# Kernel optimization log

Hardware: AMD Instinct MI355X
Metric: run time of the kernel (lower is better)

## Reference

```python
import jax, jax.numpy as jnp
import numpy as np

B, SQ, SE = 16, 1024, 1024
C_IN, C_ENC, DK, DV, H = 256, 256, 64, 64, 8
BN_EPS = 1e-5
NEG_SLOPE = 0.01  # torch LeakyReLU default


def setup_inputs() -> dict:
    key = jax.random.key(0)
    ks = jax.random.split(key, 8)
    x = jax.random.normal(ks[0], (B, SE, C_ENC), dtype=jnp.float32)
    q = jax.random.normal(ks[1], (B, SQ, C_IN), dtype=jnp.float32)
    # per-head 1x1-conv projection weights, stacked over heads
    Wq = jax.random.normal(ks[2], (H, DK, C_IN), dtype=jnp.float32) / np.sqrt(C_IN)
    Wk = jax.random.normal(ks[3], (H, DK, C_ENC), dtype=jnp.float32) / np.sqrt(C_ENC)
    Wv = jax.random.normal(ks[4], (H, DV, C_ENC), dtype=jnp.float32) / np.sqrt(C_ENC)
    # output projection (Conv1d(H*DV -> C_IN, k=1, bias=False))
    Wp = jax.random.normal(ks[5], (C_IN, H * DV), dtype=jnp.float32) / np.sqrt(H * DV)
    gamma = jax.random.normal(ks[6], (C_IN,), dtype=jnp.float32) * 0.1 + 1.0
    beta = jax.random.normal(ks[7], (C_IN,), dtype=jnp.float32) * 0.1
    return {"x": x, "q": q, "Wq": Wq, "Wk": Wk, "Wv": Wv, "Wp": Wp,
            "gamma": gamma, "beta": beta}


def reference(x, q, Wq, Wk, Wv, Wp, gamma, beta):
    # per-head Q/K/V via 1x1 conv == einsum over channel dim
    qh = jnp.einsum('bsc,hdc->bhsd', q, Wq)   # [B,H,SQ,DK]
    kh = jnp.einsum('btc,hdc->bhtd', x, Wk)   # [B,H,SE,DK]
    vh = jnp.einsum('btc,hec->bhte', x, Wv)   # [B,H,SE,DV]
    scale = 1.0 / jnp.sqrt(jnp.asarray(DK, dtype=qh.dtype))
    scores = jnp.einsum('bhsd,bhtd->bhst', qh, kh) * scale  # [B,H,SQ,SE]
    attn = jax.nn.softmax(scores, axis=-1)
    oh = jnp.einsum('bhst,bhte->bhse', attn, vh)  # [B,H,SQ,DV]
    # concat heads along feature dim (head-major order, as torch.cat over dim=2)
    o = jnp.transpose(oh, (0, 2, 1, 3)).reshape(B, SQ, H * DV)
    # LBRD projection: 1x1 conv -> BatchNorm1d (train mode: batch stats) -> LeakyReLU
    p = jnp.einsum('bsf,cf->bsc', o, Wp)  # [B,SQ,C_IN]
    mean = jnp.mean(p, axis=(0, 1))        # per-channel over (B, L)
    var = jnp.var(p, axis=(0, 1))          # biased, matching torch BN normalization
    y = (p - mean) * jax.lax.rsqrt(var + BN_EPS) * gamma + beta
    return jnp.where(y >= 0, y, NEG_SLOPE * y)
```

## Files before the change

### kernel.cpp

```cpp
#include <hip/hip_runtime.h>
#include <cstddef>

#define B_    16
#define SQ_   1024
#define SE_   1024
#define CIN_  256
#define DK_   64
#define H_    8
#define HD_   512
#define NROWS 16384
#define BN_EPS 1e-5f
#define NEG_SLOPE 0.01f

typedef __attribute__((ext_vector_type(8))) short bf16x8;
typedef __attribute__((ext_vector_type(4))) float f32x4;

#define BAR()        __builtin_amdgcn_s_barrier()
#define WAIT_LGKM0() asm volatile("s_waitcnt lgkmcnt(0)" ::: "memory")

__device__ __forceinline__ unsigned short f2bf(float f) {
    unsigned int u = __float_as_uint(f);
    return (unsigned short)((u + 0x7FFFu + ((u >> 16) & 1u)) >> 16);
}

#if __has_builtin(__builtin_amdgcn_perm)
__device__ __forceinline__ unsigned int pack_trunc(float lo, float hi) {
    return __builtin_amdgcn_perm(__float_as_uint(hi), __float_as_uint(lo), 0x07060302u);
}
#else
__device__ __forceinline__ unsigned int pack_trunc(float lo, float hi) {
    return (__float_as_uint(lo) >> 16) | (__float_as_uint(hi) & 0xFFFF0000u);
}
#endif

#if __has_builtin(__builtin_amdgcn_exp2f)
#define EXP2F(x) __builtin_amdgcn_exp2f(x)
#else
#define EXP2F(x) exp2f(x)
#endif

__device__ __forceinline__ ushort4 pack4(f32x4 v) {
    ushort4 p;
    p.x = f2bf(v[0]); p.y = f2bf(v[1]);
    p.z = f2bf(v[2]); p.w = f2bf(v[3]);
    return p;
}

__device__ __forceinline__ bf16x8 cvt8(float4 f0, float4 f1) {
    uint4 pk;
    pk.x = pack_trunc(f0.x, f0.y);
    pk.y = pack_trunc(f0.z, f0.w);
    pk.z = pack_trunc(f1.x, f1.y);
    pk.w = pack_trunc(f1.z, f1.w);
    return *(bf16x8*)&pk;
}

__global__ __launch_bounds__(256) void wcast(const float* __restrict__ Wq,
                                             const float* __restrict__ Wk,
                                             const float* __restrict__ Wv,
                                             const float* __restrict__ Wp,
                                             unsigned short* __restrict__ dWq,
                                             unsigned short* __restrict__ dWkv,
                                             unsigned short* __restrict__ dWp,
                                             float* __restrict__ stats) {
    if (blockIdx.x < 2) stats[blockIdx.x * 256 + threadIdx.x] = 0.f;
    int i = blockIdx.x * 256 + threadIdx.x;
    int which = i >> 15, off = i & 32767;
    const float* s; unsigned short* d; float sc = 1.0f;
    if (which == 0)      { s = Wq; d = dWq; sc = 0.18033688011112042f; }
    else if (which == 1) { s = Wk; d = dWkv; }
    else if (which == 2) { s = Wv; d = dWkv + 131072; }
    else                 { s = Wp; d = dWp; }
    float4 v = *(const float4*)(s + (size_t)off * 4);
    ushort4 pk;
    pk.x = f2bf(v.x * sc); pk.y = f2bf(v.y * sc);
    pk.z = f2bf(v.z * sc); pk.w = f2bf(v.w * sc);
    *(ushort4*)(d + (size_t)off * 4) = pk;
}

__global__ __launch_bounds__(256) void gemm_qkv9(const float* __restrict__ qsrc,
                                                 const float* __restrict__ xsrc,
                                                 const unsigned short* __restrict__ Wqb,
                                                 const unsigned short* __restrict__ Wkvb,
                                                 unsigned short* __restrict__ qh,
                                                 unsigned short* __restrict__ khb,
                                                 unsigned short* __restrict__ vTb) {
    __shared__ __align__(16) unsigned short smem[32768];
    unsigned short* Ws = smem;
    unsigned short* Cs = smem;

    const int tid = threadIdx.x;
    const int w = tid >> 6, l = tid & 63, lq = l >> 4, lr = l & 15;

    const int flat = blockIdx.x;
    const int xcd  = flat & 7;
    const int jj   = flat >> 3;
    const int bx   = jj % 12;
    const int by   = (jj / 12) + xcd * 16;

    const bool isQ = bx < 4;
    const bool isV = bx >= 8;
    const float* A = isQ ? qsrc : xsrc;
    const unsigned short* W = isQ ? Wqb : Wkvb;
    const int n0 = (isQ ? bx : bx - 4) * 128;
    const int m0 = by * 128;

    f32x4 acc[2][8] = {};
    float4 aA[8], aB[8];

    const float* A0 = A + (size_t)(m0 + w * 32 + lr) * 256 + lq * 8;
    const float* A1 = A + (size_t)(m0 + w * 32 + 16 + lr) * 256 + lq * 8;

#define LOAD_A(buf, kstep) do {                                              \
        buf[0] = *(const float4*)(A0 + (kstep) * 64);                        \
        buf[1] = *(const float4*)(A0 + (kstep) * 64 + 4);                    \
        buf[2] = *(const float4*)(A0 + (kstep) * 64 + 32);                   \
        buf[3] = *(const float4*)(A0 + (kstep) * 64 + 36);                   \
        buf[4] = *(const float4*)(A1 + (kstep) * 64);                        \
        buf[5] = *(const float4*)(A1 + (kstep) * 64 + 4);                    \
        buf[6] = *(const float4*)(A1 + (kstep) * 64 + 32);                   \
        buf[7] = *(const float4*)(A1 + (kstep) * 64 + 36);                   \
    } while (0)

#define QKV_STEP(buf, kstep) do {                                            \
        _Pragma("unroll")                                                    \
        for (int ks = 0; ks < 2; ++ks) {                                     \
            bf16x8 a0 = cvt8(buf[ks * 2], buf[ks * 2 + 1]);                  \
            bf16x8 a1 = cvt8(buf[4 + ks * 2], buf[4 + ks * 2 + 1]);          \
            const int colu = (kstep) * 8 + ks * 4 + lq;                      \
            const int cswz = colu ^ (lr & 7);                                \
            if (!isV) {                                                      \
                _Pragma("unroll")                                            \
                for (int j = 0; j < 8; ++j) {                                \
                    bf16x8 bb = *(bf16x8*)&Ws[((j * 16 + lr) * 32 + cswz) * 8]; \
                    acc[0][j] = __builtin_amdgcn_mfma_f32_16x16x32_bf16(bb, a0, acc[0][j], 0, 0, 0); \
                    acc[1][j] = __builtin_amdgcn_mfma_f32_16x16x32_bf16(bb, a1, acc[1][j], 0, 0, 0); \
                }                                                            \
            } else {                                                         \
                _Pragma("unroll")                                            \
                for (int j = 0; j < 8; ++j) {                                \
                    bf16x8 bb = *(bf16x8*)&Ws[((j * 16 + lr) * 32 + cswz) * 8]; \
                    acc[0][j] = __builtin_amdgcn_mfma_f32_16x16x32_bf16(a0, bb, acc[0][j], 0, 0, 0); \
                    acc[1][j] = __builtin_amdgcn_mfma_f32_16x16x32_bf16(a1, bb, acc[1][j], 0, 0, 0); \
                }                                                            \
            }                                                                \
        }                                                                    \
    } while (0)

    LOAD_A(aA, 0);

    #pragma unroll
    for (int i = 0; i < 16; ++i) {
        int u = tid + i * 256;
        int row = u >> 5, colu = u & 31;
        uint4 v = *(const uint4*)(W + (size_t)(n0 + row) * 256 + colu * 8);
        *(uint4*)&Ws[(row * 32 + (colu ^ (row & 7))) * 8] = v;
    }
    __syncthreads();

    LOAD_A(aB, 1);
    QKV_STEP(aA, 0);
    LOAD_A(aA, 2);
    QKV_STEP(aB, 1);
    LOAD_A(aB, 3);
    QKV_STEP(aA, 2);
    QKV_STEP(aB, 3);

#undef LOAD_A
#undef QKV_STEP

    __syncthreads();
    const int c16 = tid & 15;
    const int rb  = tid >> 4;
    if (!isV) {
        #pragma unroll
        for (int mf = 0; mf < 2; ++mf)
            #pragma unroll
            for (int j = 0; j < 8; ++j)
                *(ushort4*)&Cs[(w * 32 + mf * 16 + lr) * 144 + j * 16 + lq * 4] =
                    pack4(acc[mf][j]);
        __syncthreads();
        unsigned short* C = isQ ? qh : khb;
        #pragma unroll
        for (int it = 0; it < 8; ++it) {
            int r = it * 16 + rb;
            *(uint4*)(C + (size_t)(m0 + r) * 512 + n0 + c16 * 8) =
                *(const uint4*)(Cs + r * 144 + c16 * 8);
        }
    } else {
        #pragma unroll
        for (int mf = 0; mf < 2; ++mf)
            #pragma unroll
            for (int j = 0; j < 8; ++j)
                *(ushort4*)&Cs[(j * 16 + lr) * 144 + w * 32 + mf * 16 + lq * 4] =
                    pack4(acc[mf][j]);
        __syncthreads();
        const int bb = m0 >> 10, t0 = m0 & 1023;
        #pragma unroll
        for (int it = 0; it < 8; ++it) {
            int el = it * 16 + rb;
            int colv = n0 - 512 + el;
            int hh = colv >> 6, e = colv & 63;
            *(uint4*)(vTb + (size_t)((bb * 8 + hh) * 64 + e) * 1024 + t0 + c16 * 8) =
                *(const uint4*)(Cs + el * 144 + c16 * 8);
        }
    }
}

__global__ __launch_bounds__(256, 4) void attn_mfma13(const unsigned short* __restrict__ qh,
                                                      const unsigned short* __restrict__ kh,
                                                      const unsigned short* __restrict__ vT,
                                                      unsigned short* __restrict__ o) {
    __shared__ __align__(16) unsigned short Ks[64 * 64];
    __shared__ __align__(16) unsigned short Vs[64 * 64];
    __shared__ __align__(16) unsigned short Ps[4][32 * 40];

    const int tid = threadIdx.x;
    const int w = tid >> 6, l = tid & 63, lq = l >> 4, lr = l & 15;

    const int flat = blockIdx.x;
    const int xcd  = flat & 7;
    const int jj   = flat >> 3;
    const int q0   = (jj & 7) * 128;
    const int hb   = (jj >> 3) + xcd * 16;
    const int h    = hb & 7;
    const int b    = hb >> 3;

    const int swz = (lr & 7) << 3;

    bf16x8 qf[2][2];
    #pragma unroll
    for (int mm = 0; mm < 2; ++mm) {
        const unsigned short* qr =
            qh + (size_t)(b * SQ_ + q0 + w * 32 + mm * 16 + lr) * HD_ + h * DK_;
        qf[mm][0] = *(const bf16x8*)(qr + lq * 8);
        qf[mm][1] = *(const bf16x8*)(qr + 32 + lq * 8);
    }

    const unsigned short* kb = kh + (size_t)(b * SE_) * HD_ + h * DK_;
    const unsigned short* vb = vT + (size_t)((b * 8 + h) * 64) * 1024;

    const int se = tid >> 3;
    const int sc = (tid & 7) * 8;
    const int sswz = (se & 7) << 3;

    float l_i[2] = {};
    f32x4 oacc[2][4] = {};
    unsigned short* Pw = Ps[w];

    uint4 kR[2], vR[2];
    #pragma unroll
    for (int ps = 0; ps < 2; ++ps) {
        int rr = se + ps * 32;
        kR[ps] = *(const uint4*)(kb + (size_t)rr * HD_ + sc);
        vR[ps] = *(const uint4*)(vb + (size_t)rr * 1024 + sc);
    }

    for (int t0 = 0; t0 < SE_; t0 += 64) {
        BAR();
        #pragma unroll
        for (int ps = 0; ps < 2; ++ps) {
            int rr = se + ps * 32;
            int ad = ((rr * 64 + sc) ^ sswz);
            *(uint4*)&Ks[ad] = kR[ps];
            *(uint4*)&Vs[ad] = vR[ps];
        }
        if (t0 + 64 < SE_) {
            #pragma unroll
            for (int ps = 0; ps < 2; ++ps) {
                int rr = se + ps * 32;
                kR[ps] = *(const uint4*)(kb + (size_t)(t0 + 64 + rr) * HD_ + sc);
                vR[ps] = *(const uint4*)(vb + (size_t)rr * 1024 + t0 + 64 + sc);
            }
        }
        WAIT_LGKM0();
        BAR();

        f32x4 s0[2][2] = {};
        __builtin_amdgcn_s_setprio(1);
        #pragma unroll
        for (int ks = 0; ks < 2; ++ks)
            #pragma unroll
            for (int tt = 0; tt < 2; ++tt) {
                bf16x8 kf = *(bf16x8*)&Ks[((tt * 16 + lr) * 64 + ks * 32 + lq * 8) ^ swz];
                #pragma unroll
                for (int mm = 0; mm < 2; ++mm)
                    s0[tt][mm] = __builtin_amdgcn_mfma_f32_16x16x32_bf16(kf, qf[mm][ks], s0[tt][mm], 0, 0, 0);
            }
        __builtin_amdgcn_s_setprio(0);

        #pragma unroll
        for (int mm = 0; mm < 2; ++mm)
            #pragma unroll
            for (int tt = 0; tt < 2; ++tt) {
                float e0 = EXP2F(s0[tt][mm][0]);
                float e1 = EXP2F(s0[tt][mm][1]);
                float e2 = EXP2F(s0[tt][mm][2]);
                float e3 = EXP2F(s0[tt][mm][3]);
                l_i[mm] += (e0 + e1) + (e2 + e3);
                uint2 pk;
                pk.x = pack_trunc(e0, e1);
                pk.y = pack_trunc(e2, e3);
                *(uint2*)&Pw[(mm * 16 + lr) * 40 + tt * 16 + lq * 4] = pk;
            }

        f32x4 s1[2][2] = {};
        __builtin_amdgcn_s_setprio(1);
        #pragma unroll
        for (int ks = 0; ks < 2; ++ks)
            #pragma unroll
            for (int tt = 0; tt < 2; ++tt) {
                bf16x8 kf = *(bf16x8*)&Ks[(((tt + 2) * 16 + lr) * 64 + ks * 32 + lq * 8) ^ swz];
                #pragma unroll
                for (int mm = 0; mm < 2; ++mm)
                    s1[tt][mm] = __builtin_amdgcn_mfma_f32_16x16x32_bf16(kf, qf[mm][ks], s1[tt][mm], 0, 0, 0);
            }
        __builtin_amdgcn_s_setprio(0);

        asm volatile("s_waitcnt lgkmcnt(0)" ::: "memory");

        __builtin_amdgcn_s_setprio(1);
        {
            bf16x8 pf[2];
            #pragma unroll
            for (int mm = 0; mm < 2; ++mm)
                pf[mm] = *(bf16x8*)&Pw[(mm * 16 + lr) * 40 + lq * 8];
            #pragma unroll
            for (int j = 0; j < 4; ++j) {
                bf16x8 vf = *(bf16x8*)&Vs[((j * 16 + lr) * 64 + lq * 8) ^ swz];
                #pragma unroll
                for (int mm = 0; mm < 2; ++mm)
                    oacc[mm][j] = __builtin_amdgcn_mfma_f32_16x16x32_bf16(vf, pf[mm], oacc[mm][j], 0, 0, 0);
            }
        }
        __builtin_amdgcn_s_setprio(0);

        #pragma unroll
        for (int mm = 0; mm < 2; ++mm)
            #pragma unroll
            for (int tt = 0; tt < 2; ++tt) {
                float e0 = EXP2F(s1[tt][mm][0]);
                float e1 = EXP2F(s1[tt][mm][1]);
                float e2 = EXP2F(s1[tt][mm][2]);
                float e3 = EXP2F(s1[tt][mm][3]);
                l_i[mm] += (e0 + e1) + (e2 + e3);
                uint2 pk;
                pk.x = pack_trunc(e0, e1);
                pk.y = pack_trunc(e2, e3);
                *(uint2*)&Pw[(mm * 16 + lr) * 40 + tt * 16 + lq * 4] = pk;
            }

        asm volatile("s_waitcnt lgkmcnt(0)" ::: "memory");

        __builtin_amdgcn_s_setprio(1);
        {
            bf16x8 pf[2];
            #pragma unroll
            for (int mm = 0; mm < 2; ++mm)
                pf[mm] = *(bf16x8*)&Pw[(mm * 16 + lr) * 40 + lq * 8];
            #pragma unroll
            for (int j = 0; j < 4; ++j) {
                bf16x8 vf = *(bf16x8*)&Vs[((j * 16 + lr) * 64 + 32 + lq * 8) ^ swz];
                #pragma unroll
                for (int mm = 0; mm < 2; ++mm)
                    oacc[mm][j] = __builtin_amdgcn_mfma_f32_16x16x32_bf16(vf, pf[mm], oacc[mm][j], 0, 0, 0);
            }
        }
        __builtin_amdgcn_s_setprio(0);
    }

    float inv[2];
    #pragma unroll
    for (int mm = 0; mm < 2; ++mm) {
        float t = l_i[mm];
        t += __shfl_xor(t, 16);
        t += __shfl_xor(t, 32);
        inv[mm] = 1.0f / t;
    }

    #pragma unroll
    for (int mm = 0; mm < 2; ++mm)
        #pragma unroll
        for (int j = 0; j < 4; ++j) {
            f32x4 v = oacc[mm][j];
            v[0] *= inv[mm]; v[1] *= inv[mm]; v[2] *= inv[mm]; v[3] *= inv[mm];
            *(ushort4*)&o[(size_t)(b * SQ_ + q0 + w * 32 + mm * 16 + lr) * HD_ +
                          h * DK_ + j * 16 + lq * 4] = pack4(v);
        }
}

__global__ __launch_bounds__(256) void gemm_out2(const unsigned short* __restrict__ A,
                                                 const unsigned short* __restrict__ W,
                                                 float* __restrict__ C,
                                                 float* __restrict__ gsum,
                                                 float* __restrict__ gsumsq) {
    __shared__ __align__(16) unsigned short As[128 * 72];
    __shared__ __align__(16) unsigned short Ws[64 * 72];
    const int tid = threadIdx.x;
    const int w = tid >> 6, l = tid & 63, lq = l >> 4, lr = l & 15;
    const int n0 = blockIdx.x * 64, m0 = blockIdx.y * 128;
    const int K = 512;

    const int arow = tid >> 1, aoff = (tid & 1) * 32;
    const int wrow = tid >> 2, woff = (tid & 3) * 16;

    f32x4 acc[2][4] = {};
    uint4 aR[4], wR[2];

    {
        const unsigned short* Ar = A + (size_t)(m0 + arow) * K + aoff;
        #pragma unroll
        for (int c = 0; c < 4; ++c) aR[c] = *(const uint4*)(Ar + c * 8);
        const unsigned short* Wr = W + (size_t)(n0 + wrow) * K + woff;
        #pragma unroll
        for (int c = 0; c < 2; ++c) wR[c] = *(const uint4*)(Wr + c * 8);
    }

    for (int k0 = 0; k0 < K; k0 += 64) {
        BAR();
        #pragma unroll
        for (int c = 0; c < 4; ++c)
            *(uint4*)&As[arow * 72 + aoff + c * 8] = aR[c];
        #pragma unroll
        for (int c = 0; c < 2; ++c)
            *(uint4*)&Ws[wrow * 72 + woff + c * 8] = wR[c];

        if (k0 + 64 < K) {
            const unsigned short* Ar = A + (size_t)(m0 + arow) * K + k0 + 64 + aoff;
            #pragma unroll
            for (int c = 0; c < 4; ++c) aR[c] = *(const uint4*)(Ar + c * 8);
            const unsigned short* Wr = W + (size_t)(n0 + wrow) * K + k0 + 64 + woff;
            #pragma unroll
            for (int c = 0; c < 2; ++c) wR[c] = *(const uint4*)(Wr + c * 8);
        }
        WAIT_LGKM0();
        BAR();

        #pragma unroll
        for (int ks = 0; ks < 2; ++ks) {
            bf16x8 a0 = *(bf16x8*)&As[(w * 32 + lr) * 72 + ks * 32 + lq * 8];
            bf16x8 a1 = *(bf16x8*)&As[(w * 32 + 16 + lr) * 72 + ks * 32 + lq * 8];
            #pragma unroll
            for (int j = 0; j < 4; ++j) {
                bf16x8 bb = *(bf16x8*)&Ws[(j * 16 + lr) * 72 + ks * 32 + lq * 8];
                acc[0][j] = __builtin_amdgcn_mfma_f32_16x16x32_bf16(a0, bb, acc[0][j], 0, 0, 0);
                acc[1][j] = __builtin_amdgcn_mfma_f32_16x16x32_bf16(a1, bb, acc[1][j], 0, 0, 0);
            }
        }
    }

    float cs[4] = {}, cq[4] = {};
    #pragma unroll
    for (int m = 0; m < 2; ++m)
        #pragma unroll
        for (int j = 0; j < 4; ++j)
            #pragma unroll
            for (int r = 0; r < 4; ++r) {
                float v = acc[m][j][r];
                C[(size_t)(m0 + w * 32 + m * 16 + lq * 4 + r) * 256 + n0 + j * 16 + lr] = v;
                cs[j] += v;
                cq[j] += v * v;
            }
    #pragma unroll
    for (int j = 0; j < 4; ++j) {
        cs[j] += __shfl_xor(cs[j], 16); cs[j] += __shfl_xor(cs[j], 32);
        cq[j] += __shfl_xor(cq[j], 16); cq[j] += __shfl_xor(cq[j], 32);
    }
    __syncthreads();
    float* red = (float*)As;
    if (lq == 0) {
        #pragma unroll
        for (int j = 0; j < 4; ++j) {
            red[w * 128 + j * 16 + lr]      = cs[j];
            red[w * 128 + 64 + j * 16 + lr] = cq[j];
        }
    }
    __syncthreads();
    if (tid < 128) {
        int col = tid & 63, stat = tid >> 6;
        float t = red[stat * 64 + col] + red[128 + stat * 64 + col] +
                  red[256 + stat * 64 + col] + red[384 + stat * 64 + col];
        atomicAdd((stat ? gsumsq : gsum) + n0 + col, t);
    }
}

__global__ __launch_bounds__(256) void bn_norm4(const float* __restrict__ p,
                                                const float* __restrict__ gsum,
                                                const float* __restrict__ gsumsq,
                                                const float* __restrict__ gamma,
                                                const float* __restrict__ beta,
                                                float* __restrict__ out) {
    int i = blockIdx.x * 256 + threadIdx.x;
    int c0 = (i * 4) & 255;
    const float invN = 1.0f / (float)NROWS;
    float4 pv = *(const float4*)(p + (size_t)i * 4);
    float vals[4] = {pv.x, pv.y, pv.z, pv.w};
    float res[4];
    #pragma unroll
    for (int k = 0; k < 4; ++k) {
        int c = c0 + k;
        float mean = gsum[c] * invN;
        float var  = gsumsq[c] * invN - mean * mean;
        float v = (vals[k] - mean) * rsqrtf(var + BN_EPS) * gamma[c] + beta[c];
        res[k] = v >= 0.f ? v : NEG_SLOPE * v;
    }
    float4 ov = {res[0], res[1], res[2], res[3]};
    *(float4*)(out + (size_t)i * 4) = ov;
}

extern "C" void kernel_launch(void* const* d_in, const int* in_sizes, int n_in,
                              void* d_out, int out_size, void* d_ws, size_t ws_size,
                              hipStream_t stream) {
    const float* x     = (const float*)d_in[0];
    const float* q     = (const float*)d_in[1];
    const float* Wq    = (const float*)d_in[2];
    const float* Wk    = (const float*)d_in[3];
    const float* Wv    = (const float*)d_in[4];
    const float* Wp    = (const float*)d_in[5];
    const float* gamma = (const float*)d_in[6];
    const float* beta  = (const float*)d_in[7];
    float* out = (float*)d_out;

    char* base = (char*)d_ws;
    unsigned short* Wqb  = (unsigned short*)(base + 0);
    unsigned short* Wkvb = (unsigned short*)(base + 262144);
    unsigned short* Wpb  = (unsigned short*)(base + 786432);
    unsigned short* qh   = (unsigned short*)(base + 1048576);
    unsigned short* khb  = (unsigned short*)(base + 17825792);
    unsigned short* vTb  = (unsigned short*)(base + 34603008);
    unsigned short* ob   = (unsigned short*)(base + 51380224);
    float*          pbuf = (float*)        (base + 68157440);
    float*          stats= (float*)        (base + 84934656);

    wcast<<<512, 256, 0, stream>>>(Wq, Wk, Wv, Wp, Wqb, Wkvb, Wpb, stats);

    gemm_qkv9<<<1536, 256, 0, stream>>>(q, x, Wqb, Wkvb, qh, khb, vTb);

    attn_mfma13<<<1024, 256, 0, stream>>>(qh, khb, vTb, ob);

    gemm_out2<<<dim3(4, 128), 256, 0, stream>>>(ob, Wpb, pbuf, stats, stats + 256);

    bn_norm4<<<4096, 256, 0, stream>>>(pbuf, stats, stats + 256, gamma, beta, out);
}
```

Measured before the change: 222.9 us.

## Double the attention query tile with double-buffered K/V and rework the output GEMM

The attention kernel now gives each wave 64 query rows instead of 32 and launches 512 blocks instead of 1024, so each K/V tile loaded into LDS serves twice as many queries. K/V use double-buffered shared memory, which drops one barrier per iteration. The output GEMM keeps the whole 64x512 weight slice in swizzled LDS, loads A fragments straight from global into registers with ping-pong prefetch, and needs no per-k barriers. In exchange the attention kernel uses more registers and LDS and runs with fewer blocks, which can lower occupancy.

```diff
diff --git a/kernel.cpp b/kernel.cpp
--- a/kernel.cpp
+++ b/kernel.cpp
@@ -207,13 +207,13 @@
     }
 }
 
-__global__ __launch_bounds__(256, 4) void attn_mfma13(const unsigned short* __restrict__ qh,
-                                                      const unsigned short* __restrict__ kh,
-                                                      const unsigned short* __restrict__ vT,
-                                                      unsigned short* __restrict__ o) {
-    __shared__ __align__(16) unsigned short Ks[64 * 64];
-    __shared__ __align__(16) unsigned short Vs[64 * 64];
-    __shared__ __align__(16) unsigned short Ps[4][32 * 40];
+__global__ __launch_bounds__(256) void attn_mfma14(const unsigned short* __restrict__ qh,
+                                                   const unsigned short* __restrict__ kh,
+                                                   const unsigned short* __restrict__ vT,
+                                                   unsigned short* __restrict__ o) {
+    __shared__ __align__(16) unsigned short Ks[2][64 * 64];
+    __shared__ __align__(16) unsigned short Vs[2][64 * 64];
+    __shared__ __align__(16) unsigned short Ps[4][64 * 40];
 
     const int tid = threadIdx.x;
     const int w = tid >> 6, l = tid & 63, lq = l >> 4, lr = l & 15;
@@ -221,18 +221,18 @@
     const int flat = blockIdx.x;
     const int xcd  = flat & 7;
     const int jj   = flat >> 3;
-    const int q0   = (jj & 7) * 128;
-    const int hb   = (jj >> 3) + xcd * 16;
+    const int q0   = (jj & 3) * 256;
+    const int hb   = (jj >> 2) + xcd * 16;
     const int h    = hb & 7;
     const int b    = hb >> 3;
 
     const int swz = (lr & 7) << 3;
 
-    bf16x8 qf[2][2];
-    #pragma unroll
-    for (int mm = 0; mm < 2; ++mm) {
+    bf16x8 qf[4][2];
+    #pragma unroll
+    for (int mm = 0; mm < 4; ++mm) {
         const unsigned short* qr =
-            qh + (size_t)(b * SQ_ + q0 + w * 32 + mm * 16 + lr) * HD_ + h * DK_;
+            qh + (size_t)(b * SQ_ + q0 + w * 64 + mm * 16 + lr) * HD_ + h * DK_;
         qf[mm][0] = *(const bf16x8*)(qr + lq * 8);
         qf[mm][1] = *(const bf16x8*)(qr + 32 + lq * 8);
     }
@@ -244,8 +244,8 @@
     const int sc = (tid & 7) * 8;
     const int sswz = (se & 7) << 3;
 
-    float l_i[2] = {};
-    f32x4 oacc[2][4] = {};
+    float l_i[4] = {};
+    f32x4 oacc[4][4] = {};
     unsigned short* Pw = Ps[w];
 
     uint4 kR[2], vR[2];
@@ -255,42 +255,61 @@
         kR[ps] = *(const uint4*)(kb + (size_t)rr * HD_ + sc);
         vR[ps] = *(const uint4*)(vb + (size_t)rr * 1024 + sc);
     }
-
-    for (int t0 = 0; t0 < SE_; t0 += 64) {
-        BAR();
-        #pragma unroll
-        for (int ps = 0; ps < 2; ++ps) {
-            int rr = se + ps * 32;
-            int ad = ((rr * 64 + sc) ^ sswz);
-            *(uint4*)&Ks[ad] = kR[ps];
-            *(uint4*)&Vs[ad] = vR[ps];
-        }
-        if (t0 + 64 < SE_) {
+    #pragma unroll
+    for (int ps = 0; ps < 2; ++ps) {
+        int rr = se + ps * 32;
+        int ad = ((rr * 64 + sc) ^ sswz);
+        *(uint4*)&Ks[0][ad] = kR[ps];
+        *(uint4*)&Vs[0][ad] = vR[ps];
+    }
+    #pragma unroll
+    for (int ps = 0; ps < 2; ++ps) {
+        int rr = se + ps * 32;
+        kR[ps] = *(const uint4*)(kb + (size_t)(64 + rr) * HD_ + sc);
+        vR[ps] = *(const uint4*)(vb + (size_t)rr * 1024 + 64 + sc);
+    }
+    WAIT_LGKM0();
+    BAR();
+
+    for (int ti = 0; ti < 16; ++ti) {
+        unsigned short* Kc = Ks[ti & 1];
+        unsigned short* Vc = Vs[ti & 1];
+        if (ti + 1 < 16) {
+            unsigned short* Kn = Ks[(ti + 1) & 1];
+            unsigned short* Vn = Vs[(ti + 1) & 1];
             #pragma unroll
             for (int ps = 0; ps < 2; ++ps) {
                 int rr = se + ps * 32;
-                kR[ps] = *(const uint4*)(kb + (size_t)(t0 + 64 + rr) * HD_ + sc);
-                vR[ps] = *(const uint4*)(vb + (size_t)rr * 1024 + t0 + 64 + sc);
-            }
-        }
-        WAIT_LGKM0();
-        BAR();
-
-        f32x4 s0[2][2] = {};
+                int ad = ((rr * 64 + sc) ^ sswz);
+                *(uint4*)&Kn[ad] = kR[ps];
+                *(uint4*)&Vn[ad] = vR[ps];
+            }
+            if (ti + 2 < 16) {
+                int t2 = (ti + 2) * 64;
+                #pragma unroll
+                for (int ps = 0; ps < 2; ++ps) {
+                    int rr = se + ps * 32;
+                    kR[ps] = *(const uint4*)(kb + (size_t)(t2 + rr) * HD_ + sc);
+                    vR[ps] = *(const uint4*)(vb + (size_t)rr * 1024 + t2 + sc);
+                }
+            }
+        }
+
+        f32x4 s0[2][4] = {};
         __builtin_amdgcn_s_setprio(1);
         #pragma unroll
         for (int ks = 0; ks < 2; ++ks)
             #pragma unroll
             for (int tt = 0; tt < 2; ++tt) {
-                bf16x8 kf = *(bf16x8*)&Ks[((tt * 16 + lr) * 64 + ks * 32 + lq * 8) ^ swz];
+                bf16x8 kf = *(bf16x8*)&Kc[((tt * 16 + lr) * 64 + ks * 32 + lq * 8) ^ swz];
                 #pragma unroll
-                for (int mm = 0; mm < 2; ++mm)
+                for (int mm = 0; mm < 4; ++mm)
                     s0[tt][mm] = __builtin_amdgcn_mfma_f32_16x16x32_bf16(kf, qf[mm][ks], s0[tt][mm], 0, 0, 0);
             }
         __builtin_amdgcn_s_setprio(0);
 
         #pragma unroll
-        for (int mm = 0; mm < 2; ++mm)
+        for (int mm = 0; mm < 4; ++mm)
             #pragma unroll
             for (int tt = 0; tt < 2; ++tt) {
                 float e0 = EXP2F(s0[tt][mm][0]);
@@ -304,15 +323,15 @@
                 *(uint2*)&Pw[(mm * 16 + lr) * 40 + tt * 16 + lq * 4] = pk;
             }
 
-        f32x4 s1[2][2] = {};
+        f32x4 s1[2][4] = {};
         __builtin_amdgcn_s_setprio(1);
         #pragma unroll
         for (int ks = 0; ks < 2; ++ks)
             #pragma unroll
             for (int tt = 0; tt < 2; ++tt) {
-                bf16x8 kf = *(bf16x8*)&Ks[(((tt + 2) * 16 + lr) * 64 + ks * 32 + lq * 8) ^ swz];
+                bf16x8 kf = *(bf16x8*)&Kc[(((tt + 2) * 16 + lr) * 64 + ks * 32 + lq * 8) ^ swz];
                 #pragma unroll
-                for (int mm = 0; mm < 2; ++mm)
+                for (int mm = 0; mm < 4; ++mm)
                     s1[tt][mm] = __builtin_amdgcn_mfma_f32_16x16x32_bf16(kf, qf[mm][ks], s1[tt][mm], 0, 0, 0);
             }
         __builtin_amdgcn_s_setprio(0);
@@ -321,22 +340,22 @@
 
         __builtin_amdgcn_s_setprio(1);
         {
-            bf16x8 pf[2];
-            #pragma unroll
-            for (int mm = 0; mm < 2; ++mm)
+            bf16x8 pf[4];
+            #pragma unroll
+            for (int mm = 0; mm < 4; ++mm)
                 pf[mm] = *(bf16x8*)&Pw[(mm * 16 + lr) * 40 + lq * 8];
             #pragma unroll
             for (int j = 0; j < 4; ++j) {
-                bf16x8 vf = *(bf16x8*)&Vs[((j * 16 + lr) * 64 + lq * 8) ^ swz];
+                bf16x8 vf = *(bf16x8*)&Vc[((j * 16 + lr) * 64 + lq * 8) ^ swz];
                 #pragma unroll
-                for (int mm = 0; mm < 2; ++mm)
+                for (int mm = 0; mm < 4; ++mm)
                     oacc[mm][j] = __builtin_amdgcn_mfma_f32_16x16x32_bf16(vf, pf[mm], oacc[mm][j], 0, 0, 0);
             }
         }
         __builtin_amdgcn_s_setprio(0);
 
         #pragma unroll
-        for (int mm = 0; mm < 2; ++mm)
+        for (int mm = 0; mm < 4; ++mm)
             #pragma unroll
             for (int tt = 0; tt < 2; ++tt) {
                 float e0 = EXP2F(s1[tt][mm][0]);
@@ -354,24 +373,29 @@
 
         __builtin_amdgcn_s_setprio(1);
         {
-            bf16x8 pf[2];
-            #pragma unroll
-            for (int mm = 0; mm < 2; ++mm)
+            bf16x8 pf[4];
+            #pragma unroll
+            for (int mm = 0; mm < 4; ++mm)
                 pf[mm] = *(bf16x8*)&Pw[(mm * 16 + lr) * 40 + lq * 8];
             #pragma unroll
             for (int j = 0; j < 4; ++j) {
-                bf16x8 vf = *(bf16x8*)&Vs[((j * 16 + lr) * 64 + 32 + lq * 8) ^ swz];
+                bf16x8 vf = *(bf16x8*)&Vc[((j * 16 + lr) * 64 + 32 + lq * 8) ^ swz];
                 #pragma unroll
-                for (int mm = 0; mm < 2; ++mm)
+                for (int mm = 0; mm < 4; ++mm)
                     oacc[mm][j] = __builtin_amdgcn_mfma_f32_16x16x32_bf16(vf, pf[mm], oacc[mm][j], 0, 0, 0);
             }
         }
         __builtin_amdgcn_s_setprio(0);
-    }
-
-    float inv[2];
-    #pragma unroll
-    for (int mm = 0; mm < 2; ++mm) {
+
+        if (ti + 1 < 16) {
+            WAIT_LGKM0();
+            BAR();
+        }
+    }
+
+    float inv[4];
+    #pragma unroll
+    for (int mm = 0; mm < 4; ++mm) {
         float t = l_i[mm];
         t += __shfl_xor(t, 16);
         t += __shfl_xor(t, 32);
@@ -379,75 +403,78 @@
     }
 
     #pragma unroll
-    for (int mm = 0; mm < 2; ++mm)
+    for (int mm = 0; mm < 4; ++mm)
         #pragma unroll
         for (int j = 0; j < 4; ++j) {
             f32x4 v = oacc[mm][j];
             v[0] *= inv[mm]; v[1] *= inv[mm]; v[2] *= inv[mm]; v[3] *= inv[mm];
-            *(ushort4*)&o[(size_t)(b * SQ_ + q0 + w * 32 + mm * 16 + lr) * HD_ +
+            *(ushort4*)&o[(size_t)(b * SQ_ + q0 + w * 64 + mm * 16 + lr) * HD_ +
                           h * DK_ + j * 16 + lq * 4] = pack4(v);
         }
 }
 
-__global__ __launch_bounds__(256) void gemm_out2(const unsigned short* __restrict__ A,
+__global__ __launch_bounds__(256) void gemm_out3(const unsigned short* __restrict__ A,
                                                  const unsigned short* __restrict__ W,
                                                  float* __restrict__ C,
                                                  float* __restrict__ gsum,
                                                  float* __restrict__ gsumsq) {
-    __shared__ __align__(16) unsigned short As[128 * 72];
-    __shared__ __align__(16) unsigned short Ws[64 * 72];
+    __shared__ __align__(16) unsigned short Ws[32768];
     const int tid = threadIdx.x;
     const int w = tid >> 6, l = tid & 63, lq = l >> 4, lr = l & 15;
     const int n0 = blockIdx.x * 64, m0 = blockIdx.y * 128;
     const int K = 512;
 
-    const int arow = tid >> 1, aoff = (tid & 1) * 32;
-    const int wrow = tid >> 2, woff = (tid & 3) * 16;
-
     f32x4 acc[2][4] = {};
-    uint4 aR[4], wR[2];
-
-    {
-        const unsigned short* Ar = A + (size_t)(m0 + arow) * K + aoff;
-        #pragma unroll
-        for (int c = 0; c < 4; ++c) aR[c] = *(const uint4*)(Ar + c * 8);
-        const unsigned short* Wr = W + (size_t)(n0 + wrow) * K + woff;
-        #pragma unroll
-        for (int c = 0; c < 2; ++c) wR[c] = *(const uint4*)(Wr + c * 8);
-    }
-
-    for (int k0 = 0; k0 < K; k0 += 64) {
-        BAR();
-        #pragma unroll
-        for (int c = 0; c < 4; ++c)
-            *(uint4*)&As[arow * 72 + aoff + c * 8] = aR[c];
-        #pragma unroll
-        for (int c = 0; c < 2; ++c)
-            *(uint4*)&Ws[wrow * 72 + woff + c * 8] = wR[c];
-
-        if (k0 + 64 < K) {
-            const unsigned short* Ar = A + (size_t)(m0 + arow) * K + k0 + 64 + aoff;
-            #pragma unroll
-            for (int c = 0; c < 4; ++c) aR[c] = *(const uint4*)(Ar + c * 8);
-            const unsigned short* Wr = W + (size_t)(n0 + wrow) * K + k0 + 64 + woff;
-            #pragma unroll
-            for (int c = 0; c < 2; ++c) wR[c] = *(const uint4*)(Wr + c * 8);
-        }
-        WAIT_LGKM0();
-        BAR();
-
-        #pragma unroll
-        for (int ks = 0; ks < 2; ++ks) {
-            bf16x8 a0 = *(bf16x8*)&As[(w * 32 + lr) * 72 + ks * 32 + lq * 8];
-            bf16x8 a1 = *(bf16x8*)&As[(w * 32 + 16 + lr) * 72 + ks * 32 + lq * 8];
-            #pragma unroll
-            for (int j = 0; j < 4; ++j) {
-                bf16x8 bb = *(bf16x8*)&Ws[(j * 16 + lr) * 72 + ks * 32 + lq * 8];
-                acc[0][j] = __builtin_amdgcn_mfma_f32_16x16x32_bf16(a0, bb, acc[0][j], 0, 0, 0);
-                acc[1][j] = __builtin_amdgcn_mfma_f32_16x16x32_bf16(a1, bb, acc[1][j], 0, 0, 0);
-            }
-        }
-    }
+    uint4 aA[4], aB[4];
+
+    const unsigned short* A0 = A + (size_t)(m0 + w * 32 + lr) * K + lq * 8;
+    const unsigned short* A1 = A + (size_t)(m0 + w * 32 + 16 + lr) * K + lq * 8;
+
+#define LOADO(buf, kstep) do {                                               \
+        buf[0] = *(const uint4*)(A0 + (kstep) * 64);                         \
+        buf[1] = *(const uint4*)(A0 + (kstep) * 64 + 32);                    \
+        buf[2] = *(const uint4*)(A1 + (kstep) * 64);                         \
+        buf[3] = *(const uint4*)(A1 + (kstep) * 64 + 32);                    \
+    } while (0)
+
+#define OSTEP(buf, kstep) do {                                               \
+        _Pragma("unroll")                                                    \
+        for (int ks = 0; ks < 2; ++ks) {                                     \
+            bf16x8 a0 = *(bf16x8*)&buf[ks];                                  \
+            bf16x8 a1 = *(bf16x8*)&buf[2 + ks];                              \
+            const int cu = (kstep) * 8 + ks * 4 + lq;                        \
+            const int cswz = cu ^ (lr & 7);                                  \
+            _Pragma("unroll")                                                \
+            for (int j = 0; j < 4; ++j) {                                    \
+                bf16x8 bb = *(bf16x8*)&Ws[((j * 16 + lr) * 64 + cswz) * 8];  \
+                acc[0][j] = __builtin_amdgcn_mfma_f32_16x16x32_bf16(a0, bb, acc[0][j], 0, 0, 0); \
+                acc[1][j] = __builtin_amdgcn_mfma_f32_16x16x32_bf16(a1, bb, acc[1][j], 0, 0, 0); \
+            }                                                                \
+        }                                                                    \
+    } while (0)
+
+    LOADO(aA, 0);
+
+    #pragma unroll
+    for (int i = 0; i < 16; ++i) {
+        int u = tid + i * 256;
+        int row = u >> 6, cu = u & 63;
+        uint4 v = *(const uint4*)(W + (size_t)(n0 + row) * 512 + cu * 8);
+        *(uint4*)&Ws[(row * 64 + (cu ^ (row & 7))) * 8] = v;
+    }
+    __syncthreads();
+
+    LOADO(aB, 1); OSTEP(aA, 0);
+    LOADO(aA, 2); OSTEP(aB, 1);
+    LOADO(aB, 3); OSTEP(aA, 2);
+    LOADO(aA, 4); OSTEP(aB, 3);
+    LOADO(aB, 5); OSTEP(aA, 4);
+    LOADO(aA, 6); OSTEP(aB, 5);
+    LOADO(aB, 7); OSTEP(aA, 6);
+    OSTEP(aB, 7);
+
+#undef LOADO
+#undef OSTEP
 
     float cs[4] = {}, cq[4] = {};
     #pragma unroll
@@ -467,7 +494,7 @@
         cq[j] += __shfl_xor(cq[j], 16); cq[j] += __shfl_xor(cq[j], 32);
     }
     __syncthreads();
-    float* red = (float*)As;
+    float* red = (float*)Ws;
     if (lq == 0) {
         #pragma unroll
         for (int j = 0; j < 4; ++j) {
@@ -536,9 +563,9 @@
 
     gemm_qkv9<<<1536, 256, 0, stream>>>(q, x, Wqb, Wkvb, qh, khb, vTb);
 
-    attn_mfma13<<<1024, 256, 0, stream>>>(qh, khb, vTb, ob);
-
-    gemm_out2<<<dim3(4, 128), 256, 0, stream>>>(ob, Wpb, pbuf, stats, stats + 256);
+    attn_mfma14<<<512, 256, 0, stream>>>(qh, khb, vTb, ob);
+
+    gemm_out3<<<dim3(4, 128), 256, 0, stream>>>(ob, Wpb, pbuf, stats, stats + 256);
 
     bn_norm4<<<4096, 256, 0, stream>>>(pbuf, stats, stats + 256, gamma, beta, out);
 }
```

After: 225.8 us. No clear change (+1.3%).
